# Kernel tuning notes

Hardware: AMD Instinct MI355X
Metric: run time of the kernel (lower is better)

Reference implementation:

```python
import jax, jax.numpy as jnp
import numpy as np

K = 5          # top-k constant (init k)
EPSILON = 1.0  # smoothing constant (init epsilon)
N_SAMPLE = 8   # noise samples (init n_sample)


def setup_inputs() -> dict:
    key = jax.random.key(0)
    k1, k2, k3 = jax.random.split(key, 3)
    n, d, m = 64, 100000, N_SAMPLE
    s = jax.random.normal(k1, (n, d), dtype=jnp.float32)
    y = jax.random.randint(k2, (n,), 0, d, dtype=jnp.int32)
    # In torch this noise is drawn inside forward(); we materialize it as an
    # input for a deterministic reference.  shape (n_batch, d, n_sample)
    Z = jax.random.normal(k3, (n, d, m), dtype=jnp.float32)
    return {"s": s, "y": y, "Z": Z}


def reference(s, y, Z):
    """Balanced noised top-k (calibrated hinge) loss of Garcin et al., ICML'22.

    loss_i = relu(1 + smoothed_kth_max(s_i excluding class y_i) - s_{i,y_i})
    where smoothed_kth_max(v) = E_Z[ kth-largest(v + eps*Z) ] estimated with
    n_sample Gaussian draws.  Returns the batch mean.
    """
    n, d = s.shape
    # Exclude the ground-truth score from the top-k pool (s^{\y}); -inf entries
    # can never enter the top-k since k < d, so this is equivalent to dropping
    # the column while keeping a rectangular, jit-friendly shape.
    is_y = jnp.arange(d)[None, :] == y[:, None]          # (n, d)
    s_ny = jnp.where(is_y, -jnp.inf, s)                  # (n, d)
    # Perturbed scores: (n, m, d)
    pert = s_ny[:, None, :] + EPSILON * jnp.swapaxes(Z, 1, 2)
    topk_vals = jax.lax.top_k(pert, K)[0]                # (n, m, K)
    kth_smooth = topk_vals[..., K - 1].mean(axis=1)      # (n,) Monte-Carlo E[kth max]
    s_y = jnp.take_along_axis(s, y[:, None].astype(jnp.int32), axis=1)[:, 0]
    loss = jnp.maximum(1.0 + kth_smooth - s_y, 0.0)
    return loss.mean()
```

## Files before the change

### kernel.cpp

```cpp
#include <hip/hip_runtime.h>
#include <math.h>


#define KTOP 5
#define MSAMP 8
#define TPB 256
#define NCHUNKS_MAX 32

__device__ __forceinline__ void topk_insert_bl(float (&v)[KTOP], float x) {
    float n0 = __builtin_amdgcn_fmed3f(x, v[0], v[1]);
    float n1 = __builtin_amdgcn_fmed3f(x, v[1], v[2]);
    float n2 = __builtin_amdgcn_fmed3f(x, v[2], v[3]);
    float n3 = __builtin_amdgcn_fmed3f(x, v[3], v[4]);
    float n4 = fmaxf(v[4], x);
    v[0] = n0; v[1] = n1; v[2] = n2; v[3] = n3; v[4] = n4;
}

__global__ __launch_bounds__(TPB) void topk_partial(
    const float* __restrict__ s, const int* __restrict__ y,
    const float* __restrict__ Z, float* __restrict__ cand,
    int d, int nchunks, int chunk)
{
    const int i = blockIdx.x / nchunks;
    const int c = blockIdx.x % nchunks;
    const int e0 = c * chunk;
    const int e1 = min(e0 + chunk, d);
    const int yi = y[i];

    const int t = threadIdx.x;
    const int j = t & 7;
    const int eofs = t >> 3;

    const float* __restrict__ srow = s + (size_t)i * d;
    const float* __restrict__ zrow = Z + (size_t)i * d * MSAMP;

    float v[KTOP];
    #pragma unroll
    for (int q = 0; q < KTOP; ++q) v[q] = -INFINITY;

    #pragma unroll 4
    for (int e = e0 + eofs; e < e1; e += 32) {
        float sv = srow[e];
        float z  = zrow[(size_t)e * MSAMP + j];
        float x  = (e == yi) ? -INFINITY : (sv + z);
        topk_insert_bl(v, x);
    }

    #pragma unroll
    for (int off = 8; off <= 32; off <<= 1) {
        float o[KTOP];
        #pragma unroll
        for (int q = 0; q < KTOP; ++q) o[q] = __shfl_xor(v[q], off, 64);
        #pragma unroll
        for (int q = 0; q < KTOP; ++q) topk_insert_bl(v, o[q]);
    }

    __shared__ float lds[TPB / 64][MSAMP][KTOP];
    const int wave = t >> 6;
    const int lane = t & 63;
    if (lane < MSAMP) {
        #pragma unroll
        for (int q = 0; q < KTOP; ++q) lds[wave][lane][q] = v[q];
    }
    __syncthreads();

    if (t < MSAMP) {
        float f[KTOP];
        #pragma unroll
        for (int q = 0; q < KTOP; ++q) f[q] = lds[0][t][q];
        #pragma unroll
        for (int w = 1; w < TPB / 64; ++w)
            #pragma unroll
            for (int q = 0; q < KTOP; ++q) topk_insert_bl(f, lds[w][t][q]);
        float* out = cand + (((size_t)i * nchunks + c) * MSAMP + t) * KTOP;
        #pragma unroll
        for (int q = 0; q < KTOP; ++q) out[q] = f[q];
    }
}

__global__ __launch_bounds__(512) void finalize(
    const float* __restrict__ s, const int* __restrict__ y,
    const float* __restrict__ cand, float* __restrict__ out,
    int n, int d, int nchunks)
{
    const int t = threadIdx.x;
    const int i = t >> 3;
    const int j = t & 7;

    __shared__ float lsum[64];
    if (t < 64) lsum[t] = 0.0f;
    __syncthreads();

    if (i < n) {
        float v[KTOP];
        #pragma unroll
        for (int q = 0; q < KTOP; ++q) v[q] = -INFINITY;
        for (int c = 0; c < nchunks; ++c) {
            const float* p = cand + (((size_t)i * nchunks + c) * MSAMP + j) * KTOP;
            #pragma unroll
            for (int q = 0; q < KTOP; ++q) topk_insert_bl(v, p[q]);
        }
        float kth = v[0];
        kth += __shfl_xor(kth, 1, 64);
        kth += __shfl_xor(kth, 2, 64);
        kth += __shfl_xor(kth, 4, 64);
        if (j == 0) {
            float kth_smooth = kth * (1.0f / (float)MSAMP);
            float sy = s[(size_t)i * d + y[i]];
            lsum[i] = fmaxf(1.0f + kth_smooth - sy, 0.0f);
        }
    }
    __syncthreads();

    if (t < 64) {
        float x = lsum[t];
        #pragma unroll
        for (int off = 32; off >= 1; off >>= 1) x += __shfl_xor(x, off, 64);
        if (t == 0) out[0] = x / (float)n;
    }
}

extern "C" void kernel_launch(void* const* d_in, const int* in_sizes, int n_in,
                              void* d_out, int out_size, void* d_ws, size_t ws_size,
                              hipStream_t stream) {
    const float* s = (const float*)d_in[0];
    const int*   y = (const int*)d_in[1];
    const float* Z = (const float*)d_in[2];
    float* out = (float*)d_out;

    const int n = in_sizes[1];
    const int d = in_sizes[0] / n;

    int nchunks = NCHUNKS_MAX;
    while (nchunks > 1 &&
           (size_t)n * nchunks * MSAMP * KTOP * sizeof(float) > ws_size) {
        nchunks >>= 1;
    }
    const int chunk = (d + nchunks - 1) / nchunks;
    float* cand = (float*)d_ws;

    hipLaunchKernelGGL(topk_partial, dim3(n * nchunks), dim3(TPB), 0, stream,
                       s, y, Z, cand, d, nchunks, chunk);
    hipLaunchKernelGGL(finalize, dim3(1), dim3(n * MSAMP), 0, stream,
                       s, y, cand, out, n, d, nchunks);
}
```

Baseline: 54.34 us.

## Parallelize final top-k merge across rows and add separate mean kernel

Replaces the single-block finalize kernel with a per-row merge kernel (one block per row, threads striding over chunks) followed by a tiny 64-thread mean kernel. It also raises the main loop unroll to 8 and rounds the chunk size up to a multiple of 32. The aim is to remove the serial per-thread merge over all chunks in the finalize step, at the cost of an extra kernel launch and a workspace slot for per-row losses.

Measured after the change: 44.42 us, median of 2. 18.3% less time.

```diff
diff --git a/kernel.cpp b/kernel.cpp
--- a/kernel.cpp
+++ b/kernel.cpp
@@ -5,7 +5,7 @@
 #define KTOP 5
 #define MSAMP 8
 #define TPB 256
-#define NCHUNKS_MAX 32
+#define NCHUNKS 32
 
 __device__ __forceinline__ void topk_insert_bl(float (&v)[KTOP], float x) {
     float n0 = __builtin_amdgcn_fmed3f(x, v[0], v[1]);
@@ -38,7 +38,7 @@
     #pragma unroll
     for (int q = 0; q < KTOP; ++q) v[q] = -INFINITY;
 
-    #pragma unroll 4
+    #pragma unroll 8
     for (int e = e0 + eofs; e < e1; e += 32) {
         float sv = srow[e];
         float z  = zrow[(size_t)e * MSAMP + j];
@@ -78,46 +78,74 @@
     }
 }
 
-__global__ __launch_bounds__(512) void finalize(
+__global__ __launch_bounds__(TPB) void row_loss(
     const float* __restrict__ s, const int* __restrict__ y,
-    const float* __restrict__ cand, float* __restrict__ out,
-    int n, int d, int nchunks)
+    const float* __restrict__ cand, float* __restrict__ rloss,
+    int d, int nchunks)
 {
+    const int i = blockIdx.x;
     const int t = threadIdx.x;
-    const int i = t >> 3;
     const int j = t & 7;
+    const int wave = t >> 6;
+    const int lane = t & 63;
 
-    __shared__ float lsum[64];
-    if (t < 64) lsum[t] = 0.0f;
-    __syncthreads();
+    float v[KTOP];
+    #pragma unroll
+    for (int q = 0; q < KTOP; ++q) v[q] = -INFINITY;
 
-    if (i < n) {
-        float v[KTOP];
+    for (int c = t >> 3; c < nchunks; c += TPB / MSAMP) {
+        const float* p = cand + (((size_t)i * nchunks + c) * MSAMP + j) * KTOP;
         #pragma unroll
-        for (int q = 0; q < KTOP; ++q) v[q] = -INFINITY;
-        for (int c = 0; c < nchunks; ++c) {
-            const float* p = cand + (((size_t)i * nchunks + c) * MSAMP + j) * KTOP;
-            #pragma unroll
-            for (int q = 0; q < KTOP; ++q) topk_insert_bl(v, p[q]);
-        }
-        float kth = v[0];
-        kth += __shfl_xor(kth, 1, 64);
-        kth += __shfl_xor(kth, 2, 64);
-        kth += __shfl_xor(kth, 4, 64);
-        if (j == 0) {
-            float kth_smooth = kth * (1.0f / (float)MSAMP);
-            float sy = s[(size_t)i * d + y[i]];
-            lsum[i] = fmaxf(1.0f + kth_smooth - sy, 0.0f);
-        }
+        for (int q = 0; q < KTOP; ++q) topk_insert_bl(v, p[q]);
+    }
+
+    #pragma unroll
+    for (int off = 8; off <= 32; off <<= 1) {
+        float o[KTOP];
+        #pragma unroll
+        for (int q = 0; q < KTOP; ++q) o[q] = __shfl_xor(v[q], off, 64);
+        #pragma unroll
+        for (int q = 0; q < KTOP; ++q) topk_insert_bl(v, o[q]);
+    }
+
+    __shared__ float lds[TPB / 64][MSAMP][KTOP];
+    __shared__ float kth_j[MSAMP];
+    if (lane < MSAMP) {
+        #pragma unroll
+        for (int q = 0; q < KTOP; ++q) lds[wave][lane][q] = v[q];
     }
     __syncthreads();
 
-    if (t < 64) {
-        float x = lsum[t];
+    if (t < MSAMP) {
+        float f[KTOP];
         #pragma unroll
-        for (int off = 32; off >= 1; off >>= 1) x += __shfl_xor(x, off, 64);
-        if (t == 0) out[0] = x / (float)n;
+        for (int q = 0; q < KTOP; ++q) f[q] = lds[0][t][q];
+        #pragma unroll
+        for (int w = 1; w < TPB / 64; ++w)
+            #pragma unroll
+            for (int q = 0; q < KTOP; ++q) topk_insert_bl(f, lds[w][t][q]);
+        kth_j[t] = f[0];
     }
+    __syncthreads();
+
+    if (t == 0) {
+        float sum = 0.0f;
+        #pragma unroll
+        for (int jj = 0; jj < MSAMP; ++jj) sum += kth_j[jj];
+        float kth_smooth = sum * (1.0f / (float)MSAMP);
+        float sy = s[(size_t)i * d + y[i]];
+        rloss[i] = fmaxf(1.0f + kth_smooth - sy, 0.0f);
+    }
+}
+
+__global__ __launch_bounds__(64) void mean_loss(
+    const float* __restrict__ rloss, float* __restrict__ out, int n)
+{
+    const int t = threadIdx.x;
+    float x = (t < n) ? rloss[t] : 0.0f;
+    #pragma unroll
+    for (int off = 32; off >= 1; off >>= 1) x += __shfl_xor(x, off, 64);
+    if (t == 0) out[0] = x / (float)n;
 }
 
 extern "C" void kernel_launch(void* const* d_in, const int* in_sizes, int n_in,
@@ -131,16 +159,21 @@
     const int n = in_sizes[1];
     const int d = in_sizes[0] / n;
 
-    int nchunks = NCHUNKS_MAX;
+    int nchunks = NCHUNKS;
     while (nchunks > 1 &&
-           (size_t)n * nchunks * MSAMP * KTOP * sizeof(float) > ws_size) {
+           (size_t)n * nchunks * MSAMP * KTOP * sizeof(float) + n * sizeof(float)
+               > ws_size) {
         nchunks >>= 1;
     }
-    const int chunk = (d + nchunks - 1) / nchunks;
-    float* cand = (float*)d_ws;
+    int chunk = (d + nchunks - 1) / nchunks;
+    chunk = (chunk + 31) & ~31;
+    float* cand  = (float*)d_ws;
+    float* rloss = cand + (size_t)n * nchunks * MSAMP * KTOP;
 
     hipLaunchKernelGGL(topk_partial, dim3(n * nchunks), dim3(TPB), 0, stream,
                        s, y, Z, cand, d, nchunks, chunk);
-    hipLaunchKernelGGL(finalize, dim3(1), dim3(n * MSAMP), 0, stream,
-                       s, y, cand, out, n, d, nchunks);
+    hipLaunchKernelGGL(row_loss, dim3(n), dim3(TPB), 0, stream,
+                       s, y, cand, rloss, d, nchunks);
+    hipLaunchKernelGGL(mean_loss, dim3(1), dim3(64), 0, stream,
+                       rloss, out, n);
 }
```
